# Performance work log

Measured on AMD Instinct MI355X. Metric: run time of the kernel, lower is better.

The kernel has to match this reference:

```python
import jax, jax.numpy as jnp
import numpy as np

NUM_HEADS = 12
EPSILON = 1e-6
SCORE_SCALE = 1.0


def setup_inputs() -> dict:
    key = jax.random.key(0)
    ks = jax.random.split(key, 5)
    B, L, E = 2, 2048, 768
    x = jax.random.normal(ks[0], (B, L, E), dtype=jnp.float32)
    attention_mask = jnp.ones((B, L), dtype=jnp.int32)
    # linear params (lecun-ish scale)
    Wqkv = jax.random.normal(ks[1], (E, 3 * E), dtype=jnp.float32) / np.sqrt(E)
    bqkv = jnp.zeros((3 * E,), dtype=jnp.float32)
    Wout = jax.random.normal(ks[2], (E, E), dtype=jnp.float32) / np.sqrt(E)
    bout = jnp.zeros((E,), dtype=jnp.float32)
    return {"x": x, "attention_mask": attention_mask, "Wqkv": Wqkv,
            "bqkv": bqkv, "Wout": Wout, "bout": bout}


def reference(x, attention_mask, Wqkv, bqkv, Wout, bout):
    B, L, E = x.shape
    H = NUM_HEADS
    D = E // H
    qkv = x @ Wqkv + bqkv                      # [B,L,3E]
    q, k, v = jnp.split(qkv, 3, axis=-1)
    q = q.reshape(B, L, H, D).transpose(0, 2, 1, 3)  # [B,H,L,D]
    k = k.reshape(B, L, H, D).transpose(0, 2, 1, 3)
    v = v.reshape(B, L, H, D).transpose(0, 2, 1, 3)

    dot = jnp.einsum('bhid,bhjd->bhij', q, k)        # [B,H,L,L]
    q_sq = jnp.sum(q * q, axis=-1)[..., :, None]     # [B,H,L,1]
    k_sq = jnp.sum(k * k, axis=-1)[..., None, :]     # [B,H,1,L]
    scores = (dot * dot) / (q_sq + k_sq - 2.0 * dot + EPSILON)
    scores = scores * SCORE_SCALE

    pad = attention_mask[:, None, None, :]           # [B,1,1,L]
    scores = jnp.where(pad == 1, scores, jnp.finfo(scores.dtype).min)

    attn = jax.nn.softmax(scores, axis=-1)
    out = jnp.einsum('bhij,bhjd->bhid', attn, v)     # [B,H,L,D]
    out = out.transpose(0, 2, 1, 3).reshape(B, L, E)
    return out @ Wout + bout
```

## Files before the change

### kernel.cpp

```cpp
#include <hip/hip_runtime.h>
#include <hip/hip_bf16.h>
#include <cstdint>
#include <cstddef>


typedef __bf16 bf16_t;
typedef __bf16 bf16x8 __attribute__((ext_vector_type(8)));
typedef __bf16 bf16x4 __attribute__((ext_vector_type(4)));
typedef float floatx4 __attribute__((ext_vector_type(4)));

#define DEVI static __device__ __forceinline__

#define Bc 2
#define Lc 2048
#define Ec 768
#define Hc 12
#define Dc 64
#define N3c 2304
#define Mc 4096
#define ROWSc (Bc * Hc * Lc)

DEVI void glds16(const bf16_t* g, bf16_t* l) {
  __builtin_amdgcn_global_load_lds(
      (const __attribute__((address_space(1))) void*)g,
      (__attribute__((address_space(3))) void*)l, 16, 0, 0);
}

__global__ __launch_bounds__(256) void k_prep(
    const float* __restrict__ x, bf16_t* __restrict__ xb,
    const float* __restrict__ Wqkv, bf16_t* __restrict__ WqT,
    const float* __restrict__ Wout, bf16_t* __restrict__ WoT) {
  __shared__ float tile[32][33];
  const int bid = blockIdx.x, tid = threadIdx.x;
  if (bid < 3072) {
    const int i = (bid * 256 + tid) * 4;
    float4 v = *(const float4*)(x + i);
    bf16x4 o;
    o[0] = (bf16_t)v.x; o[1] = (bf16_t)v.y; o[2] = (bf16_t)v.z; o[3] = (bf16_t)v.w;
    *(bf16x4*)(xb + i) = o;
    return;
  }
  const float* in; bf16_t* out; int C, local;
  if (bid < 4800) { local = bid - 3072; in = Wqkv; out = WqT; C = N3c; }
  else            { local = bid - 4800; in = Wout; out = WoT; C = Ec;  }
  const int R = Ec;
  const int nbx = C / 32;
  const int c0 = (local % nbx) * 32, r0 = (local / nbx) * 32;
  const int tx = tid & 31, ty = tid >> 5;
  #pragma unroll
  for (int i = 0; i < 32; i += 8)
    tile[ty + i][tx] = in[(size_t)(r0 + ty + i) * C + c0 + tx];
  __syncthreads();
  #pragma unroll
  for (int i = 0; i < 32; i += 8)
    out[(size_t)(c0 + ty + i) * R + r0 + tx] = (bf16_t)tile[tx][ty + i];
}


DEVI void gemm_core(const bf16_t* __restrict__ A, const bf16_t* __restrict__ Bt,
                    bf16_t* lA, bf16_t* lB, int m0, int n0, floatx4 (&acc)[4][4]) {
  const int tid = threadIdx.x, wave = tid >> 6, lane = tid & 63;
  const int wm = (wave >> 1) * 64, wn = (wave & 1) * 64;
  const int lrow = lane >> 2, lseg = lane & 3;
  const int quad = lane >> 4, r16 = lane & 15;
  for (int kk = 0; kk < 768; kk += 32) {
    glds16(A  + (size_t)(m0 + wave * 32      + lrow) * 768 + kk + lseg * 8, lA + (wave * 32) * 32);
    glds16(A  + (size_t)(m0 + wave * 32 + 16 + lrow) * 768 + kk + lseg * 8, lA + (wave * 32 + 16) * 32);
    glds16(Bt + (size_t)(n0 + wave * 32      + lrow) * 768 + kk + lseg * 8, lB + (wave * 32) * 32);
    glds16(Bt + (size_t)(n0 + wave * 32 + 16 + lrow) * 768 + kk + lseg * 8, lB + (wave * 32 + 16) * 32);
    __syncthreads();
    bf16x8 af[4], bv[4];
    #pragma unroll
    for (int mi = 0; mi < 4; mi++)
      af[mi] = *(const bf16x8*)(lA + (wm + mi * 16 + r16) * 32 + quad * 8);
    #pragma unroll
    for (int ni = 0; ni < 4; ni++)
      bv[ni] = *(const bf16x8*)(lB + (wn + ni * 16 + r16) * 32 + quad * 8);
    #pragma unroll
    for (int mi = 0; mi < 4; mi++)
      #pragma unroll
      for (int ni = 0; ni < 4; ni++)
        acc[mi][ni] = __builtin_amdgcn_mfma_f32_16x16x32_bf16(af[mi], bv[ni], acc[mi][ni], 0, 0, 0);
    __syncthreads();
  }
}

__global__ __launch_bounds__(256) void k_gemm_qkv(
    const bf16_t* __restrict__ A, const bf16_t* __restrict__ Bt,
    const float* __restrict__ bias,
    bf16_t* __restrict__ Qo, bf16_t* __restrict__ Ko, bf16_t* __restrict__ Vo) {
  __shared__ bf16_t lA[128 * 32];
  __shared__ bf16_t lB[128 * 32];
  const int m0 = blockIdx.y * 128, n0 = blockIdx.x * 128;
  const int tid = threadIdx.x, wave = tid >> 6, lane = tid & 63;
  const int wm = (wave >> 1) * 64, wn = (wave & 1) * 64;
  const int quad = lane >> 4, r16 = lane & 15;
  floatx4 acc[4][4] = {};
  gemm_core(A, Bt, lA, lB, m0, n0, acc);

  const int sec = n0 / 768;
  bf16_t* dst = (sec == 0) ? Qo : ((sec == 1) ? Ko : Vo);
  #pragma unroll
  for (int ni = 0; ni < 4; ni++) {
    const int n = n0 + wn + ni * 16 + r16;
    const int nn = n - sec * 768;
    const int h = nn >> 6, d = nn & 63;
    const float bvs = bias[n];
    #pragma unroll
    for (int mi = 0; mi < 4; mi++) {
      #pragma unroll
      for (int reg = 0; reg < 4; reg++) {
        const int m = m0 + wm + mi * 16 + quad * 4 + reg;
        const int b = m >> 11, l = m & 2047;
        const float v = acc[mi][ni][reg] + bvs;
        dst[(((size_t)(b * Hc + h)) * Lc + l) * Dc + d] = (bf16_t)v;
      }
    }
  }
}

__global__ __launch_bounds__(256) void k_gemm_out(
    const bf16_t* __restrict__ A, const bf16_t* __restrict__ Bt,
    const float* __restrict__ bias, float* __restrict__ out) {
  __shared__ bf16_t lA[128 * 32];
  __shared__ bf16_t lB[128 * 32];
  const int m0 = blockIdx.y * 128, n0 = blockIdx.x * 128;
  const int tid = threadIdx.x, wave = tid >> 6, lane = tid & 63;
  const int wm = (wave >> 1) * 64, wn = (wave & 1) * 64;
  const int quad = lane >> 4, r16 = lane & 15;
  floatx4 acc[4][4] = {};
  gemm_core(A, Bt, lA, lB, m0, n0, acc);
  #pragma unroll
  for (int ni = 0; ni < 4; ni++) {
    const int n = n0 + wn + ni * 16 + r16;
    const float bvs = bias[n];
    #pragma unroll
    for (int mi = 0; mi < 4; mi++) {
      #pragma unroll
      for (int reg = 0; reg < 4; reg++) {
        const int m = m0 + wm + mi * 16 + quad * 4 + reg;
        out[(size_t)m * Ec + n] = acc[mi][ni][reg] + bvs;
      }
    }
  }
}

__global__ __launch_bounds__(256) void k_prep2(
    const bf16_t* __restrict__ Q, const bf16_t* __restrict__ K,
    const int* __restrict__ mask,
    float* __restrict__ qsq, float* __restrict__ ksq,
    float* __restrict__ mbias,
    const bf16_t* __restrict__ V, bf16_t* __restrict__ VT) {
  __shared__ bf16_t tb[64][72];
  const int bid = blockIdx.x, tid = threadIdx.x;
  if (bid < 192) {
    const int row = bid * 256 + tid;
    const bf16x8* q = (const bf16x8*)(Q + (size_t)row * 64);
    const bf16x8* k = (const bf16x8*)(K + (size_t)row * 64);
    float sq = 0.f, sk = 0.f;
    #pragma unroll
    for (int c = 0; c < 8; c++) {
      bf16x8 vq = q[c], vk = k[c];
      #pragma unroll
      for (int j = 0; j < 8; j++) {
        float a = (float)vq[j]; sq += a * a;
        float b = (float)vk[j]; sk += b * b;
      }
    }
    qsq[row] = sq;
    ksq[row] = sk + 1e-6f;
    const int bh = row >> 11, l = row & 2047;
    if (bh == 0 || bh == Hc) {
      const int b = bh / Hc;
      mbias[b * Lc + l] = (mask[b * Lc + l] == 1) ? 0.f : -1e30f;
    }
    return;
  }
  const int gid = bid - 192;
  const int bh = gid >> 5, j0 = (gid & 31) * 64;
  const bf16_t* Vh = V + ((size_t)bh * Lc) * Dc;
  bf16_t* VTh = VT + ((size_t)bh * Dc) * Lc;
  #pragma unroll
  for (int it = 0; it < 2; ++it) {
    int c = tid + it * 256;
    int j = c >> 3, seg = c & 7;
    *(bf16x8*)&tb[j][seg * 8] = *(const bf16x8*)(Vh + (size_t)(j0 + j) * 64 + seg * 8);
  }
  __syncthreads();
  #pragma unroll
  for (int it = 0; it < 2; ++it) {
    int c = tid + it * 256;
    int d = c >> 3, jseg = c & 7;
    bf16x8 o;
    #pragma unroll
    for (int u = 0; u < 8; u++) o[u] = tb[jseg * 8 + u][d];
    *(bf16x8*)(VTh + (size_t)d * Lc + j0 + jseg * 8) = o;
  }
}

__global__ __launch_bounds__(256) void k_attn(
    const bf16_t* __restrict__ Q, const bf16_t* __restrict__ K,
    const bf16_t* __restrict__ VT, const float* __restrict__ qsq,
    const float* __restrict__ ksq, const float* __restrict__ mbias,
    bf16_t* __restrict__ AO) {
  __shared__ bf16_t lK[2][4096];
  __shared__ bf16_t lV[2][4096];
  __shared__ bf16_t lP[4][16 * 72];
  const int gid0 = blockIdx.x;
  const int gid = (gid0 & 7) * 96 + (gid0 >> 3);
  const int bh = gid >> 5, qt = gid & 31;
  const int b = bh / Hc;
  const int h = bh - b * Hc;
  const int tid = threadIdx.x, wave = tid >> 6, lane = tid & 63;
  const int quad = lane >> 4, r16 = lane & 15;
  const int q0 = qt * 64 + wave * 16;
  const bf16_t* Qh = Q + ((size_t)bh * Lc) * Dc;
  const bf16_t* Kh = K + ((size_t)bh * Lc) * Dc;
  const bf16_t* VTh = VT + ((size_t)bh * Dc) * Lc;
  const float* qsqh = qsq + bh * Lc;
  const float* ksqh = ksq + bh * Lc;
  const float* mbb = mbias + b * Lc;
  bf16_t* myP = &lP[wave][0];

  const int p0 = wave * 64 + lane;
  const int srow = p0 >> 3;
  const int sj = (p0 & 7) ^ (srow & 7);
  const bf16_t* kg0 = Kh + (size_t)srow * 64 + sj * 8;
  const bf16_t* kg1 = kg0 + 32 * 64;
  const bf16_t* vg0 = VTh + (size_t)srow * Lc + sj * 8;
  const bf16_t* vg1 = vg0 + 32 * Lc;
  const int ld0 = wave * 64 * 8, ld1 = (256 + wave * 64) * 8;

  const int sl0 = ((quad ^ (r16 & 7)) * 8);
  const int sl1 = sl0 ^ 32;

  bf16x8 qf0 = *(const bf16x8*)(Qh + (size_t)(q0 + r16) * 64 + quad * 8);
  bf16x8 qf1 = *(const bf16x8*)(Qh + (size_t)(q0 + r16) * 64 + 32 + quad * 8);
  const float qs = qsqh[q0 + r16];
  float mi = -1e30f;
  float li = 0.f;
  floatx4 of[4] = {};

  glds16(kg0, &lK[0][ld0]);
  glds16(kg1, &lK[0][ld1]);
  glds16(vg0, &lV[0][ld0]);
  glds16(vg1, &lV[0][ld1]);
  kg0 += 4096; kg1 += 4096; vg0 += 64; vg1 += 64;
  float4 ks4[4], mb4[4];
  #pragma unroll
  for (int c = 0; c < 4; c++) {
    ks4[c] = *(const float4*)(ksqh + c * 16 + quad * 4);
    mb4[c] = *(const float4*)(mbb + c * 16 + quad * 4);
  }
  __syncthreads();

  const int nt = Lc / 64;
  for (int t = 0; t < nt; t++) {
    const int cur = t & 1;
    const bool more = (t + 1 < nt);
    if (more) {
      const int nxt = cur ^ 1;
      glds16(kg0, &lK[nxt][ld0]);
      glds16(kg1, &lK[nxt][ld1]);
      glds16(vg0, &lV[nxt][ld0]);
      glds16(vg1, &lV[nxt][ld1]);
      kg0 += 4096; kg1 += 4096; vg0 += 64; vg1 += 64;
    }
    float4 ks4n[4], mb4n[4];
    if (more) {
      const int ktn = (t + 1) * 64;
      #pragma unroll
      for (int c = 0; c < 4; c++) {
        ks4n[c] = *(const float4*)(ksqh + ktn + c * 16 + quad * 4);
        mb4n[c] = *(const float4*)(mbb + ktn + c * 16 + quad * 4);
      }
    }
    floatx4 dot[4];
    #pragma unroll
    for (int c = 0; c < 4; c++) {
      const int rbase = (c * 16 + r16) * 64;
      bf16x8 kf0 = *(const bf16x8*)(&lK[cur][rbase + sl0]);
      bf16x8 kf1 = *(const bf16x8*)(&lK[cur][rbase + sl1]);
      floatx4 a = {};
      a = __builtin_amdgcn_mfma_f32_16x16x32_bf16(kf0, qf0, a, 0, 0, 0);
      a = __builtin_amdgcn_mfma_f32_16x16x32_bf16(kf1, qf1, a, 0, 0, 0);
      dot[c] = a;
    }
    float rmax = -1e30f;
    #pragma unroll
    for (int c = 0; c < 4; c++) {
      #pragma unroll
      for (int reg = 0; reg < 4; reg++) {
        const float dd = dot[c][reg];
        const float kss = ((const float*)&ks4[c])[reg];
        const float mbv = ((const float*)&mb4[c])[reg];
        const float den = __builtin_fmaf(dd, -2.f, qs + kss);
        const float sc = __builtin_fmaf((dd * 1.44269504f) * dd,
                                        __builtin_amdgcn_rcpf(den), mbv);
        dot[c][reg] = sc;
        rmax = fmaxf(rmax, sc);
      }
    }
    if (!__all(rmax <= mi + 11.5416f)) {
      float rg = fmaxf(rmax, __shfl_xor(rmax, 16));
      rg = fmaxf(rg, __shfl_xor(rg, 32));
      const float mnew = fmaxf(mi, rg);
      const float alpha = exp2f(mi - mnew);
      li *= alpha;
      #pragma unroll
      for (int t4 = 0; t4 < 4; t4++) {
        #pragma unroll
        for (int reg = 0; reg < 4; reg++) of[t4][reg] *= alpha;
      }
      mi = mnew;
    }
    float psum = 0.f;
    #pragma unroll
    for (int c = 0; c < 4; c++) {
      bf16x4 pk;
      #pragma unroll
      for (int reg = 0; reg < 4; reg++) {
        const float p = exp2f(dot[c][reg] - mi);
        psum += p;
        pk[reg] = (bf16_t)p;
      }
      *(bf16x4*)(myP + r16 * 72 + c * 16 + quad * 4) = pk;
    }
    li += psum;
    bf16x8 pf0 = *(const bf16x8*)(myP + r16 * 72 + quad * 8);
    bf16x8 pf1 = *(const bf16x8*)(myP + r16 * 72 + 32 + quad * 8);
    #pragma unroll
    for (int t4 = 0; t4 < 4; t4++) {
      const int rbase = (t4 * 16 + r16) * 64;
      bf16x8 vf0 = *(const bf16x8*)(&lV[cur][rbase + sl0]);
      bf16x8 vf1 = *(const bf16x8*)(&lV[cur][rbase + sl1]);
      of[t4] = __builtin_amdgcn_mfma_f32_16x16x32_bf16(vf0, pf0, of[t4], 0, 0, 0);
      of[t4] = __builtin_amdgcn_mfma_f32_16x16x32_bf16(vf1, pf1, of[t4], 0, 0, 0);
    }
    if (more) {
      #pragma unroll
      for (int c = 0; c < 4; c++) { ks4[c] = ks4n[c]; mb4[c] = mb4n[c]; }
    }
    __syncthreads();
  }
  li += __shfl_xor(li, 16);
  li += __shfl_xor(li, 32);
  const float inv = (li > 0.f) ? __builtin_amdgcn_rcpf(li) : 0.f;
  bf16_t* aor = AO + ((size_t)(b * Lc + q0 + r16)) * Ec + h * 64;
  #pragma unroll
  for (int t4 = 0; t4 < 4; t4++) {
    bf16x4 o;
    #pragma unroll
    for (int reg = 0; reg < 4; reg++) o[reg] = (bf16_t)(of[t4][reg] * inv);
    *(bf16x4*)(aor + t4 * 16 + quad * 4) = o;
  }
}


extern "C" void kernel_launch(void* const* d_in, const int* in_sizes, int n_in,
                              void* d_out, int out_size, void* d_ws, size_t ws_size,
                              hipStream_t stream) {
  const float* x    = (const float*)d_in[0];
  const int*   mask = (const int*)d_in[1];
  const float* Wqkv = (const float*)d_in[2];
  const float* bqkv = (const float*)d_in[3];
  const float* Wout = (const float*)d_in[4];
  const float* bout = (const float*)d_in[5];
  float* out = (float*)d_out;

  auto al = [](size_t x) { return (x + 255) & ~(size_t)255; };
  char* ws = (char*)d_ws;
  size_t off = 0;
  auto carve = [&](size_t bytes) -> char* {
    char* p = ws + off;
    off += al(bytes);
    return p;
  };
  bf16_t* WoT = (bf16_t*)carve((size_t)Ec * Ec * 2);
  bf16_t* Qb  = (bf16_t*)carve((size_t)ROWSc * Dc * 2);
  bf16_t* Kb  = (bf16_t*)carve((size_t)ROWSc * Dc * 2);
  bf16_t* VTb = (bf16_t*)carve((size_t)ROWSc * Dc * 2);
  bf16_t* AOb = (bf16_t*)carve((size_t)Mc * Ec * 2);
  float*  qsq = (float*)carve((size_t)ROWSc * 4);
  float*  ksq = (float*)carve((size_t)ROWSc * 4);
  float*  mbias = (float*)carve((size_t)Bc * Lc * 4);
  const size_t uni = off;
  bf16_t* xb  = (bf16_t*)(ws + uni);
  bf16_t* WqT = (bf16_t*)(ws + uni + al((size_t)Mc * Ec * 2));
  bf16_t* Vb  = (bf16_t*)(ws + uni + al((size_t)Mc * Ec * 2) + al((size_t)N3c * Ec * 2));
  (void)in_sizes; (void)n_in; (void)out_size; (void)ws_size;

  k_prep<<<5376, 256, 0, stream>>>(x, xb, Wqkv, WqT, Wout, WoT);
  k_gemm_qkv<<<dim3(N3c / 128, Mc / 128), 256, 0, stream>>>(xb, WqT, bqkv, Qb, Kb, Vb);
  k_prep2<<<960, 256, 0, stream>>>(Qb, Kb, mask, qsq, ksq, mbias, Vb, VTb);
  k_attn<<<dim3(ROWSc / 64), 256, 0, stream>>>(Qb, Kb, VTb, qsq, ksq, mbias, AOb);
  k_gemm_out<<<dim3(Ec / 128, Mc / 128), 256, 0, stream>>>(AOb, WoT, bout, out);
}
```

Measured before the change: 210.4 us.

## Single-buffer V tile via register staging and swizzle P tile to raise occupancy

The attention kernel drops the double-buffered V LDS tile. The next V tile is now loaded into registers during compute and written to LDS after the PV MMAs, which needs an extra barrier per iteration. The P scratch tile loses its padding and uses an XOR swizzle instead, and launch bounds request 5 blocks per SM. Less shared memory per block is meant to allow more resident blocks, at the cost of an added synchronization and register pressure from the staged V data.

```diff
diff --git a/kernel.cpp b/kernel.cpp
--- a/kernel.cpp
+++ b/kernel.cpp
@@ -198,14 +198,14 @@
   }
 }
 
-__global__ __launch_bounds__(256) void k_attn(
+__global__ __launch_bounds__(256, 5) void k_attn(
     const bf16_t* __restrict__ Q, const bf16_t* __restrict__ K,
     const bf16_t* __restrict__ VT, const float* __restrict__ qsq,
     const float* __restrict__ ksq, const float* __restrict__ mbias,
     bf16_t* __restrict__ AO) {
   __shared__ bf16_t lK[2][4096];
-  __shared__ bf16_t lV[2][4096];
-  __shared__ bf16_t lP[4][16 * 72];
+  __shared__ bf16_t lV[4096];
+  __shared__ bf16_t lP[4][16 * 64];
   const int gid0 = blockIdx.x;
   const int gid = (gid0 & 7) * 96 + (gid0 >> 3);
   const int bh = gid >> 5, qt = gid & 31;
@@ -234,6 +234,8 @@
   const int sl0 = ((quad ^ (r16 & 7)) * 8);
   const int sl1 = sl0 ^ 32;
 
+  const int pswz = r16 & 7;
+
   bf16x8 qf0 = *(const bf16x8*)(Qh + (size_t)(q0 + r16) * 64 + quad * 8);
   bf16x8 qf1 = *(const bf16x8*)(Qh + (size_t)(q0 + r16) * 64 + 32 + quad * 8);
   const float qs = qsqh[q0 + r16];
@@ -243,8 +245,8 @@
 
   glds16(kg0, &lK[0][ld0]);
   glds16(kg1, &lK[0][ld1]);
-  glds16(vg0, &lV[0][ld0]);
-  glds16(vg1, &lV[0][ld1]);
+  glds16(vg0, &lV[ld0]);
+  glds16(vg1, &lV[ld1]);
   kg0 += 4096; kg1 += 4096; vg0 += 64; vg1 += 64;
   float4 ks4[4], mb4[4];
   #pragma unroll
@@ -258,13 +260,14 @@
   for (int t = 0; t < nt; t++) {
     const int cur = t & 1;
     const bool more = (t + 1 < nt);
+    bf16x8 vr0, vr1;
     if (more) {
-      const int nxt = cur ^ 1;
-      glds16(kg0, &lK[nxt][ld0]);
-      glds16(kg1, &lK[nxt][ld1]);
-      glds16(vg0, &lV[nxt][ld0]);
-      glds16(vg1, &lV[nxt][ld1]);
-      kg0 += 4096; kg1 += 4096; vg0 += 64; vg1 += 64;
+      glds16(kg0, &lK[cur ^ 1][ld0]);
+      glds16(kg1, &lK[cur ^ 1][ld1]);
+      kg0 += 4096; kg1 += 4096;
+      vr0 = *(const bf16x8*)vg0;
+      vr1 = *(const bf16x8*)vg1;
+      vg0 += 64; vg1 += 64;
     }
     float4 ks4n[4], mb4n[4];
     if (more) {
@@ -324,24 +327,28 @@
         psum += p;
         pk[reg] = (bf16_t)p;
       }
-      *(bf16x4*)(myP + r16 * 72 + c * 16 + quad * 4) = pk;
+      const int jw = (2 * c + (quad >> 1)) ^ pswz;
+      *(bf16x4*)(myP + r16 * 64 + jw * 8 + (quad & 1) * 4) = pk;
     }
     li += psum;
-    bf16x8 pf0 = *(const bf16x8*)(myP + r16 * 72 + quad * 8);
-    bf16x8 pf1 = *(const bf16x8*)(myP + r16 * 72 + 32 + quad * 8);
+    bf16x8 pf0 = *(const bf16x8*)(myP + r16 * 64 + (quad ^ pswz) * 8);
+    bf16x8 pf1 = *(const bf16x8*)(myP + r16 * 64 + ((4 + quad) ^ pswz) * 8);
     #pragma unroll
     for (int t4 = 0; t4 < 4; t4++) {
       const int rbase = (t4 * 16 + r16) * 64;
-      bf16x8 vf0 = *(const bf16x8*)(&lV[cur][rbase + sl0]);
-      bf16x8 vf1 = *(const bf16x8*)(&lV[cur][rbase + sl1]);
+      bf16x8 vf0 = *(const bf16x8*)(&lV[rbase + sl0]);
+      bf16x8 vf1 = *(const bf16x8*)(&lV[rbase + sl1]);
       of[t4] = __builtin_amdgcn_mfma_f32_16x16x32_bf16(vf0, pf0, of[t4], 0, 0, 0);
       of[t4] = __builtin_amdgcn_mfma_f32_16x16x32_bf16(vf1, pf1, of[t4], 0, 0, 0);
     }
+    __syncthreads();
     if (more) {
+      *(bf16x8*)(&lV[p0 * 8]) = vr0;
+      *(bf16x8*)(&lV[(p0 + 256) * 8]) = vr1;
+      __syncthreads();
       #pragma unroll
       for (int c = 0; c < 4; c++) { ks4[c] = ks4n[c]; mb4[c] = mb4n[c]; }
     }
-    __syncthreads();
   }
   li += __shfl_xor(li, 16);
   li += __shfl_xor(li, 32);
```

Result: slower. 223.4 us (+6.2%).

## Split attention over key range (flash-decoding style) and merge partials

Applied to the files above, without the earlier changes.

The attention kernel now splits the key sequence into S chunks via a second grid dimension, writing unnormalized fp32 partial outputs plus running max and sum per row. A new merge kernel combines the partials with log-sum-exp weighting and writes the bf16 attention output. The aim is to raise the block count from 768 to 1536 so the GPU is better filled, at the cost of extra fp32 traffic and an added kernel launch. The P staging buffer also moves from padded rows to an XOR-swizzled layout to avoid LDS bank conflicts without padding.

```diff
diff --git a/kernel.cpp b/kernel.cpp
--- a/kernel.cpp
+++ b/kernel.cpp
@@ -202,15 +202,16 @@
     const bf16_t* __restrict__ Q, const bf16_t* __restrict__ K,
     const bf16_t* __restrict__ VT, const float* __restrict__ qsq,
     const float* __restrict__ ksq, const float* __restrict__ mbias,
-    bf16_t* __restrict__ AO) {
+    float* __restrict__ Op, float* __restrict__ Mp, float* __restrict__ Lp,
+    int nS) {
   __shared__ bf16_t lK[2][4096];
   __shared__ bf16_t lV[2][4096];
-  __shared__ bf16_t lP[4][16 * 72];
+  __shared__ bf16_t lP[4][16 * 64];
   const int gid0 = blockIdx.x;
   const int gid = (gid0 & 7) * 96 + (gid0 >> 3);
+  const int s = blockIdx.y;
   const int bh = gid >> 5, qt = gid & 31;
   const int b = bh / Hc;
-  const int h = bh - b * Hc;
   const int tid = threadIdx.x, wave = tid >> 6, lane = tid & 63;
   const int quad = lane >> 4, r16 = lane & 15;
   const int q0 = qt * 64 + wave * 16;
@@ -222,17 +223,22 @@
   const float* mbb = mbias + b * Lc;
   bf16_t* myP = &lP[wave][0];
 
+  const int kt_lo = (32 * s) / nS * 64;
+  const int kt_hi = (32 * (s + 1)) / nS * 64;
+  const int nt = (kt_hi - kt_lo) >> 6;
+
   const int p0 = wave * 64 + lane;
   const int srow = p0 >> 3;
   const int sj = (p0 & 7) ^ (srow & 7);
-  const bf16_t* kg0 = Kh + (size_t)srow * 64 + sj * 8;
+  const bf16_t* kg0 = Kh + (size_t)(kt_lo + srow) * 64 + sj * 8;
   const bf16_t* kg1 = kg0 + 32 * 64;
-  const bf16_t* vg0 = VTh + (size_t)srow * Lc + sj * 8;
+  const bf16_t* vg0 = VTh + (size_t)srow * Lc + kt_lo + sj * 8;
   const bf16_t* vg1 = vg0 + 32 * Lc;
   const int ld0 = wave * 64 * 8, ld1 = (256 + wave * 64) * 8;
 
   const int sl0 = ((quad ^ (r16 & 7)) * 8);
   const int sl1 = sl0 ^ 32;
+  const int pswz = r16 & 7;
 
   bf16x8 qf0 = *(const bf16x8*)(Qh + (size_t)(q0 + r16) * 64 + quad * 8);
   bf16x8 qf1 = *(const bf16x8*)(Qh + (size_t)(q0 + r16) * 64 + 32 + quad * 8);
@@ -249,12 +255,11 @@
   float4 ks4[4], mb4[4];
   #pragma unroll
   for (int c = 0; c < 4; c++) {
-    ks4[c] = *(const float4*)(ksqh + c * 16 + quad * 4);
-    mb4[c] = *(const float4*)(mbb + c * 16 + quad * 4);
+    ks4[c] = *(const float4*)(ksqh + kt_lo + c * 16 + quad * 4);
+    mb4[c] = *(const float4*)(mbb + kt_lo + c * 16 + quad * 4);
   }
   __syncthreads();
 
-  const int nt = Lc / 64;
   for (int t = 0; t < nt; t++) {
     const int cur = t & 1;
     const bool more = (t + 1 < nt);
@@ -268,7 +273,7 @@
     }
     float4 ks4n[4], mb4n[4];
     if (more) {
-      const int ktn = (t + 1) * 64;
+      const int ktn = kt_lo + (t + 1) * 64;
       #pragma unroll
       for (int c = 0; c < 4; c++) {
         ks4n[c] = *(const float4*)(ksqh + ktn + c * 16 + quad * 4);
@@ -324,11 +329,12 @@
         psum += p;
         pk[reg] = (bf16_t)p;
       }
-      *(bf16x4*)(myP + r16 * 72 + c * 16 + quad * 4) = pk;
+      const int jw = (2 * c + (quad >> 1)) ^ pswz;
+      *(bf16x4*)(myP + r16 * 64 + jw * 8 + (quad & 1) * 4) = pk;
     }
     li += psum;
-    bf16x8 pf0 = *(const bf16x8*)(myP + r16 * 72 + quad * 8);
-    bf16x8 pf1 = *(const bf16x8*)(myP + r16 * 72 + 32 + quad * 8);
+    bf16x8 pf0 = *(const bf16x8*)(myP + r16 * 64 + (quad ^ pswz) * 8);
+    bf16x8 pf1 = *(const bf16x8*)(myP + r16 * 64 + ((4 + quad) ^ pswz) * 8);
     #pragma unroll
     for (int t4 = 0; t4 < 4; t4++) {
       const int rbase = (t4 * 16 + r16) * 64;
@@ -345,15 +351,37 @@
   }
   li += __shfl_xor(li, 16);
   li += __shfl_xor(li, 32);
-  const float inv = (li > 0.f) ? __builtin_amdgcn_rcpf(li) : 0.f;
-  bf16_t* aor = AO + ((size_t)(b * Lc + q0 + r16)) * Ec + h * 64;
-  #pragma unroll
-  for (int t4 = 0; t4 < 4; t4++) {
-    bf16x4 o;
-    #pragma unroll
-    for (int reg = 0; reg < 4; reg++) o[reg] = (bf16_t)(of[t4][reg] * inv);
-    *(bf16x4*)(aor + t4 * 16 + quad * 4) = o;
-  }
+  const size_t idx = (size_t)s * ROWSc + (size_t)bh * Lc + q0 + r16;
+  #pragma unroll
+  for (int t4 = 0; t4 < 4; t4++)
+    *(float4*)(Op + idx * 64 + t4 * 16 + quad * 4) =
+        make_float4(of[t4][0], of[t4][1], of[t4][2], of[t4][3]);
+  if (lane < 16) { Mp[idx] = mi; Lp[idx] = li; }
+}
+
+__global__ __launch_bounds__(256) void k_merge(
+    const float* __restrict__ Op, const float* __restrict__ Mp,
+    const float* __restrict__ Lp, bf16_t* __restrict__ AO, int nS) {
+  const int t = blockIdx.x * 256 + threadIdx.x;
+  const int row = t >> 4, dc = (t & 15) * 4;
+  float mmax = -1e30f;
+  for (int s = 0; s < nS; s++) mmax = fmaxf(mmax, Mp[(size_t)s * ROWSc + row]);
+  float L = 0.f;
+  float o0 = 0.f, o1 = 0.f, o2 = 0.f, o3 = 0.f;
+  for (int s = 0; s < nS; s++) {
+    const size_t idx = (size_t)s * ROWSc + row;
+    const float w = exp2f(Mp[idx] - mmax);
+    L += w * Lp[idx];
+    const float4 v = *(const float4*)(Op + idx * 64 + dc);
+    o0 += w * v.x; o1 += w * v.y; o2 += w * v.z; o3 += w * v.w;
+  }
+  const float inv = (L > 0.f) ? __builtin_amdgcn_rcpf(L) : 0.f;
+  const int bh = row >> 11, l = row & 2047;
+  const int b = bh / Hc, h = bh - b * Hc;
+  bf16x4 o;
+  o[0] = (bf16_t)(o0 * inv); o[1] = (bf16_t)(o1 * inv);
+  o[2] = (bf16_t)(o2 * inv); o[3] = (bf16_t)(o3 * inv);
+  *(bf16x4*)(AO + ((size_t)(b * Lc + l)) * Ec + h * 64 + dc) = o;
 }
 
 
@@ -388,11 +416,24 @@
   bf16_t* xb  = (bf16_t*)(ws + uni);
   bf16_t* WqT = (bf16_t*)(ws + uni + al((size_t)Mc * Ec * 2));
   bf16_t* Vb  = (bf16_t*)(ws + uni + al((size_t)Mc * Ec * 2) + al((size_t)N3c * Ec * 2));
-  (void)in_sizes; (void)n_in; (void)out_size; (void)ws_size;
+  const size_t ph1 = al((size_t)Mc * Ec * 2) + al((size_t)N3c * Ec * 2) + al((size_t)ROWSc * Dc * 2);
+  auto ph2 = [&](int S) {
+    return al((size_t)S * ROWSc * Dc * 4) + 2 * al((size_t)S * ROWSc * 4);
+  };
+  int S = 1;
+  {
+    size_t need = uni + (ph1 > ph2(2) ? ph1 : ph2(2));
+    if (need <= ws_size) S = 2;
+  }
+  float* Op = (float*)(ws + uni);
+  float* Mp = (float*)(ws + uni + al((size_t)S * ROWSc * Dc * 4));
+  float* Lp = (float*)(ws + uni + al((size_t)S * ROWSc * Dc * 4) + al((size_t)S * ROWSc * 4));
+  (void)in_sizes; (void)n_in; (void)out_size;
 
   k_prep<<<5376, 256, 0, stream>>>(x, xb, Wqkv, WqT, Wout, WoT);
   k_gemm_qkv<<<dim3(N3c / 128, Mc / 128), 256, 0, stream>>>(xb, WqT, bqkv, Qb, Kb, Vb);
   k_prep2<<<960, 256, 0, stream>>>(Qb, Kb, mask, qsq, ksq, mbias, Vb, VTb);
-  k_attn<<<dim3(ROWSc / 64), 256, 0, stream>>>(Qb, Kb, VTb, qsq, ksq, mbias, AOb);
+  k_attn<<<dim3(ROWSc / 64, S), 256, 0, stream>>>(Qb, Kb, VTb, qsq, ksq, mbias, Op, Mp, Lp, S);
+  k_merge<<<ROWSc * 16 / 256, 256, 0, stream>>>(Op, Mp, Lp, AOb, S);
   k_gemm_out<<<dim3(Ec / 128, Mc / 128), 256, 0, stream>>>(AOb, WoT, bout, out);
 }
```

New measurement: 230.7 us. +9.6%, slower.

## Write V transposed from QKV GEMM epilogue, swizzle P buffer, add MFMA priority

Applied to the files above, without the earlier changes.

The QKV GEMM epilogue now writes the V section directly in [B,H,D,L] layout with 4-element vector stores, so the transpose pass in k_prep2 and the intermediate V buffer go away. The attention kernel folds q_sq into the k_sq vector once per tile, which saves one add per score. It also switches the P staging buffer from padded rows to an XOR-swizzled layout and raises wave priority around the MFMA blocks. The transposed V stores are strided by L, which may make the GEMM epilogue writes less coalesced.

```diff
diff --git a/kernel.cpp b/kernel.cpp
--- a/kernel.cpp
+++ b/kernel.cpp
@@ -88,7 +88,7 @@
 __global__ __launch_bounds__(256) void k_gemm_qkv(
     const bf16_t* __restrict__ A, const bf16_t* __restrict__ Bt,
     const float* __restrict__ bias,
-    bf16_t* __restrict__ Qo, bf16_t* __restrict__ Ko, bf16_t* __restrict__ Vo) {
+    bf16_t* __restrict__ Qo, bf16_t* __restrict__ Ko, bf16_t* __restrict__ VTo) {
   __shared__ bf16_t lA[128 * 32];
   __shared__ bf16_t lB[128 * 32];
   const int m0 = blockIdx.y * 128, n0 = blockIdx.x * 128;
@@ -99,21 +99,41 @@
   gemm_core(A, Bt, lA, lB, m0, n0, acc);
 
   const int sec = n0 / 768;
-  bf16_t* dst = (sec == 0) ? Qo : ((sec == 1) ? Ko : Vo);
-  #pragma unroll
-  for (int ni = 0; ni < 4; ni++) {
-    const int n = n0 + wn + ni * 16 + r16;
-    const int nn = n - sec * 768;
-    const int h = nn >> 6, d = nn & 63;
-    const float bvs = bias[n];
-    #pragma unroll
-    for (int mi = 0; mi < 4; mi++) {
-      #pragma unroll
-      for (int reg = 0; reg < 4; reg++) {
-        const int m = m0 + wm + mi * 16 + quad * 4 + reg;
+  if (sec < 2) {
+    bf16_t* dst = (sec == 0) ? Qo : Ko;
+    #pragma unroll
+    for (int ni = 0; ni < 4; ni++) {
+      const int n = n0 + wn + ni * 16 + r16;
+      const int nn = n - sec * 768;
+      const int h = nn >> 6, d = nn & 63;
+      const float bvs = bias[n];
+      #pragma unroll
+      for (int mi = 0; mi < 4; mi++) {
+        #pragma unroll
+        for (int reg = 0; reg < 4; reg++) {
+          const int m = m0 + wm + mi * 16 + quad * 4 + reg;
+          const int b = m >> 11, l = m & 2047;
+          const float v = acc[mi][ni][reg] + bvs;
+          dst[(((size_t)(b * Hc + h)) * Lc + l) * Dc + d] = (bf16_t)v;
+        }
+      }
+    }
+  } else {
+    #pragma unroll
+    for (int ni = 0; ni < 4; ni++) {
+      const int n = n0 + wn + ni * 16 + r16;
+      const int nn = n - 1536;
+      const int h = nn >> 6, d = nn & 63;
+      const float bvs = bias[n];
+      #pragma unroll
+      for (int mi = 0; mi < 4; mi++) {
+        const int m = m0 + wm + mi * 16 + quad * 4;
         const int b = m >> 11, l = m & 2047;
-        const float v = acc[mi][ni][reg] + bvs;
-        dst[(((size_t)(b * Hc + h)) * Lc + l) * Dc + d] = (bf16_t)v;
+        bf16x4 o;
+        #pragma unroll
+        for (int reg = 0; reg < 4; reg++)
+          o[reg] = (bf16_t)(acc[mi][ni][reg] + bvs);
+        *(bf16x4*)(VTo + (((size_t)(b * Hc + h)) * Dc + d) * Lc + l) = o;
       }
     }
   }
@@ -149,52 +169,26 @@
     const bf16_t* __restrict__ Q, const bf16_t* __restrict__ K,
     const int* __restrict__ mask,
     float* __restrict__ qsq, float* __restrict__ ksq,
-    float* __restrict__ mbias,
-    const bf16_t* __restrict__ V, bf16_t* __restrict__ VT) {
-  __shared__ bf16_t tb[64][72];
-  const int bid = blockIdx.x, tid = threadIdx.x;
-  if (bid < 192) {
-    const int row = bid * 256 + tid;
-    const bf16x8* q = (const bf16x8*)(Q + (size_t)row * 64);
-    const bf16x8* k = (const bf16x8*)(K + (size_t)row * 64);
-    float sq = 0.f, sk = 0.f;
-    #pragma unroll
-    for (int c = 0; c < 8; c++) {
-      bf16x8 vq = q[c], vk = k[c];
-      #pragma unroll
-      for (int j = 0; j < 8; j++) {
-        float a = (float)vq[j]; sq += a * a;
-        float b = (float)vk[j]; sk += b * b;
-      }
-    }
-    qsq[row] = sq;
-    ksq[row] = sk + 1e-6f;
-    const int bh = row >> 11, l = row & 2047;
-    if (bh == 0 || bh == Hc) {
-      const int b = bh / Hc;
-      mbias[b * Lc + l] = (mask[b * Lc + l] == 1) ? 0.f : -1e30f;
-    }
-    return;
-  }
-  const int gid = bid - 192;
-  const int bh = gid >> 5, j0 = (gid & 31) * 64;
-  const bf16_t* Vh = V + ((size_t)bh * Lc) * Dc;
-  bf16_t* VTh = VT + ((size_t)bh * Dc) * Lc;
-  #pragma unroll
-  for (int it = 0; it < 2; ++it) {
-    int c = tid + it * 256;
-    int j = c >> 3, seg = c & 7;
-    *(bf16x8*)&tb[j][seg * 8] = *(const bf16x8*)(Vh + (size_t)(j0 + j) * 64 + seg * 8);
-  }
-  __syncthreads();
-  #pragma unroll
-  for (int it = 0; it < 2; ++it) {
-    int c = tid + it * 256;
-    int d = c >> 3, jseg = c & 7;
-    bf16x8 o;
-    #pragma unroll
-    for (int u = 0; u < 8; u++) o[u] = tb[jseg * 8 + u][d];
-    *(bf16x8*)(VTh + (size_t)d * Lc + j0 + jseg * 8) = o;
+    float* __restrict__ mbias) {
+  const int row = blockIdx.x * 256 + threadIdx.x;
+  const bf16x8* q = (const bf16x8*)(Q + (size_t)row * 64);
+  const bf16x8* k = (const bf16x8*)(K + (size_t)row * 64);
+  float sq = 0.f, sk = 0.f;
+  #pragma unroll
+  for (int c = 0; c < 8; c++) {
+    bf16x8 vq = q[c], vk = k[c];
+    #pragma unroll
+    for (int j = 0; j < 8; j++) {
+      float a = (float)vq[j]; sq += a * a;
+      float b = (float)vk[j]; sk += b * b;
+    }
+  }
+  qsq[row] = sq;
+  ksq[row] = sk + 1e-6f;
+  const int bh = row >> 11, l = row & 2047;
+  if (bh == 0 || bh == Hc) {
+    const int b = bh / Hc;
+    mbias[b * Lc + l] = (mask[b * Lc + l] == 1) ? 0.f : -1e30f;
   }
 }
 
@@ -205,7 +199,7 @@
     bf16_t* __restrict__ AO) {
   __shared__ bf16_t lK[2][4096];
   __shared__ bf16_t lV[2][4096];
-  __shared__ bf16_t lP[4][16 * 72];
+  __shared__ bf16_t lP[4][16 * 64];
   const int gid0 = blockIdx.x;
   const int gid = (gid0 & 7) * 96 + (gid0 >> 3);
   const int bh = gid >> 5, qt = gid & 31;
@@ -233,6 +227,7 @@
 
   const int sl0 = ((quad ^ (r16 & 7)) * 8);
   const int sl1 = sl0 ^ 32;
+  const int pswz = r16 & 7;
 
   bf16x8 qf0 = *(const bf16x8*)(Qh + (size_t)(q0 + r16) * 64 + quad * 8);
   bf16x8 qf1 = *(const bf16x8*)(Qh + (size_t)(q0 + r16) * 64 + 32 + quad * 8);
@@ -249,7 +244,8 @@
   float4 ks4[4], mb4[4];
   #pragma unroll
   for (int c = 0; c < 4; c++) {
-    ks4[c] = *(const float4*)(ksqh + c * 16 + quad * 4);
+    float4 kv = *(const float4*)(ksqh + c * 16 + quad * 4);
+    ks4[c] = make_float4(kv.x + qs, kv.y + qs, kv.z + qs, kv.w + qs);
     mb4[c] = *(const float4*)(mbb + c * 16 + quad * 4);
   }
   __syncthreads();
@@ -276,6 +272,7 @@
       }
     }
     floatx4 dot[4];
+    __builtin_amdgcn_s_setprio(1);
     #pragma unroll
     for (int c = 0; c < 4; c++) {
       const int rbase = (c * 16 + r16) * 64;
@@ -286,15 +283,16 @@
       a = __builtin_amdgcn_mfma_f32_16x16x32_bf16(kf1, qf1, a, 0, 0, 0);
       dot[c] = a;
     }
+    __builtin_amdgcn_s_setprio(0);
     float rmax = -1e30f;
     #pragma unroll
     for (int c = 0; c < 4; c++) {
       #pragma unroll
       for (int reg = 0; reg < 4; reg++) {
         const float dd = dot[c][reg];
-        const float kss = ((const float*)&ks4[c])[reg];
+        const float qks = ((const float*)&ks4[c])[reg];
         const float mbv = ((const float*)&mb4[c])[reg];
-        const float den = __builtin_fmaf(dd, -2.f, qs + kss);
+        const float den = __builtin_fmaf(dd, -2.f, qks);
         const float sc = __builtin_fmaf((dd * 1.44269504f) * dd,
                                         __builtin_amdgcn_rcpf(den), mbv);
         dot[c][reg] = sc;
@@ -324,11 +322,13 @@
         psum += p;
         pk[reg] = (bf16_t)p;
       }
-      *(bf16x4*)(myP + r16 * 72 + c * 16 + quad * 4) = pk;
+      const int jw = (2 * c + (quad >> 1)) ^ pswz;
+      *(bf16x4*)(myP + r16 * 64 + jw * 8 + (quad & 1) * 4) = pk;
     }
     li += psum;
-    bf16x8 pf0 = *(const bf16x8*)(myP + r16 * 72 + quad * 8);
-    bf16x8 pf1 = *(const bf16x8*)(myP + r16 * 72 + 32 + quad * 8);
+    bf16x8 pf0 = *(const bf16x8*)(myP + r16 * 64 + (quad ^ pswz) * 8);
+    bf16x8 pf1 = *(const bf16x8*)(myP + r16 * 64 + ((4 + quad) ^ pswz) * 8);
+    __builtin_amdgcn_s_setprio(1);
     #pragma unroll
     for (int t4 = 0; t4 < 4; t4++) {
       const int rbase = (t4 * 16 + r16) * 64;
@@ -337,9 +337,14 @@
       of[t4] = __builtin_amdgcn_mfma_f32_16x16x32_bf16(vf0, pf0, of[t4], 0, 0, 0);
       of[t4] = __builtin_amdgcn_mfma_f32_16x16x32_bf16(vf1, pf1, of[t4], 0, 0, 0);
     }
+    __builtin_amdgcn_s_setprio(0);
     if (more) {
       #pragma unroll
-      for (int c = 0; c < 4; c++) { ks4[c] = ks4n[c]; mb4[c] = mb4n[c]; }
+      for (int c = 0; c < 4; c++) {
+        ks4[c] = make_float4(ks4n[c].x + qs, ks4n[c].y + qs,
+                             ks4n[c].z + qs, ks4n[c].w + qs);
+        mb4[c] = mb4n[c];
+      }
     }
     __syncthreads();
   }
@@ -387,12 +392,11 @@
   const size_t uni = off;
   bf16_t* xb  = (bf16_t*)(ws + uni);
   bf16_t* WqT = (bf16_t*)(ws + uni + al((size_t)Mc * Ec * 2));
-  bf16_t* Vb  = (bf16_t*)(ws + uni + al((size_t)Mc * Ec * 2) + al((size_t)N3c * Ec * 2));
   (void)in_sizes; (void)n_in; (void)out_size; (void)ws_size;
 
   k_prep<<<5376, 256, 0, stream>>>(x, xb, Wqkv, WqT, Wout, WoT);
-  k_gemm_qkv<<<dim3(N3c / 128, Mc / 128), 256, 0, stream>>>(xb, WqT, bqkv, Qb, Kb, Vb);
-  k_prep2<<<960, 256, 0, stream>>>(Qb, Kb, mask, qsq, ksq, mbias, Vb, VTb);
+  k_gemm_qkv<<<dim3(N3c / 128, Mc / 128), 256, 0, stream>>>(xb, WqT, bqkv, Qb, Kb, VTb);
+  k_prep2<<<192, 256, 0, stream>>>(Qb, Kb, mask, qsq, ksq, mbias);
   k_attn<<<dim3(ROWSc / 64), 256, 0, stream>>>(Qb, Kb, VTb, qsq, ksq, mbias, AOb);
   k_gemm_out<<<dim3(Ec / 128, Mc / 128), 256, 0, stream>>>(AOb, WoT, bout, out);
 }
```

Result: no change. 211.4 us, median of 3 (+0.5%).
